# Optimization experiments

Measured on AMD Instinct MI355X. Metric: run time of the kernel, lower is better.

Reference implementation:

```python
import jax, jax.numpy as jnp
import numpy as np

N, E, F_IN, H, L = 50000, 800000, 128, 256, 3


def setup_inputs() -> dict:
    key = jax.random.key(0)
    ks = jax.random.split(key, 6)
    s = 0.05  # keep activations well-scaled through 3 residual layers
    return {
        "x": jax.random.normal(ks[0], (N, F_IN), jnp.float32),
        "edge_index": jax.random.randint(ks[1], (2, E), 0, N, dtype=jnp.int32),
        "Wp": jax.random.normal(ks[2], (H, F_IN), jnp.float32) * s,
        "bp": jnp.zeros((H,), jnp.float32),
        "Wl": jax.random.normal(ks[3], (L, H, H), jnp.float32) * s,
        "bl": jnp.zeros((L, H), jnp.float32),
        "Wr": jax.random.normal(ks[4], (L, H, H), jnp.float32) * s,
        "gamma": jnp.ones((L, H), jnp.float32),
        "beta": jnp.zeros((L, H), jnp.float32),
    }


def _layernorm(x, g, b, eps=1e-5):
    mu = jnp.mean(x, axis=-1, keepdims=True)
    var = jnp.var(x, axis=-1, keepdims=True)
    return (x - mu) * jax.lax.rsqrt(var + eps) * g + b


def reference(x, edge_index, Wp, bp, Wl, bl, Wr, gamma, beta):
    n = x.shape[0]
    src, dst = edge_index[0], edge_index[1]
    # input projection + ReLU
    h = jax.nn.relu(x @ Wp.T + bp)  # [N, H]
    # mean-aggregation normalizer (PyG SAGEConv 'mean'): zero-degree nodes -> 0
    deg = jax.ops.segment_sum(jnp.ones_like(dst, jnp.float32), dst, num_segments=n)
    inv_deg = (1.0 / jnp.maximum(deg, 1.0))[:, None]  # [N, 1]
    num_layers = Wl.shape[0]
    for i in range(num_layers):
        res = h
        # SAGEConv: lin_l(mean of source-neighbor messages) + lin_r(self)
        agg = jax.ops.segment_sum(h[src], dst, num_segments=n) * inv_deg  # [N, H]
        h = agg @ Wl[i].T + bl[i] + h @ Wr[i].T
        # LayerNorm -> ReLU -> (dropout: eval-mode identity) -> residual
        h = jax.nn.relu(_layernorm(h, gamma[i], beta[i])) + res
    return h
```

## Files before the change

kernel.cpp:

```cpp
#include <hip/hip_runtime.h>

#define NN 50000
#define EE 800000
#define FIN 128
#define HH 256
#define NL 3

#define BM 64
#define BK 32
#define ABYTES (BM*BK*2)
#define BBYTES (HH*BK*2)
#define TILEB  (ABYTES + BBYTES)
#define CSRB   782

typedef __bf16 bf16x8 __attribute__((ext_vector_type(8)));
typedef float  f32x4  __attribute__((ext_vector_type(4)));
typedef unsigned short u16x8 __attribute__((ext_vector_type(8)));

__device__ __forceinline__ float bf2f(unsigned short u){
    union { unsigned int i; float f; } v; v.i = ((unsigned int)u) << 16; return v.f;
}
__device__ __forceinline__ unsigned short f2bf(float f){
    union { float f; unsigned int i; } v; v.f = f;
    unsigned int r = v.i + 0x7FFF + ((v.i >> 16) & 1);
    return (unsigned short)(r >> 16);
}
__device__ __forceinline__ void gload16(const void* g, void* s){
    __builtin_amdgcn_global_load_lds(
        (const __attribute__((address_space(1))) void*)g,
        (__attribute__((address_space(3))) void*)s, 16, 0, 0);
}
__device__ __forceinline__ int permslot(int n){
    return (n & ~63) | ((n & 3) << 4) | ((n >> 2) & 15);
}

__global__ void k_zero_i32(int* __restrict__ p, int n){
    int i = blockIdx.x*256 + threadIdx.x;
    if (i < n) p[i] = 0;
}
__global__ void k_count_deg(const int* __restrict__ dst, int* __restrict__ deg){
    int i = blockIdx.x*256 + threadIdx.x;
    if (i < EE) atomicAdd(&deg[dst[i]], 1);
}
__global__ void k_block_sum(const int* __restrict__ deg, int* __restrict__ bsum){
    __shared__ int s[1024];
    int i = blockIdx.x*1024 + threadIdx.x;
    s[threadIdx.x] = (i < NN) ? deg[i] : 0;
    __syncthreads();
    for (int o = 512; o > 0; o >>= 1){
        if (threadIdx.x < o) s[threadIdx.x] += s[threadIdx.x + o];
        __syncthreads();
    }
    if (threadIdx.x == 0) bsum[blockIdx.x] = s[0];
}
__global__ void k_make_off(const int* __restrict__ deg, const int* __restrict__ bsum,
                           int nb, int* __restrict__ off, int* __restrict__ pos,
                           float* __restrict__ invd){
    __shared__ int s[1024];
    __shared__ int base;
    int t = threadIdx.x;
    if (t < 64){
        int v = (t < blockIdx.x && t < nb) ? bsum[t] : 0;
        #pragma unroll
        for (int m = 1; m <= 32; m <<= 1) v += __shfl_xor(v, m);
        if (t == 0) base = v;
    }
    int i = blockIdx.x*1024 + t;
    int v0 = (i < NN) ? deg[i] : 0;
    s[t] = v0; __syncthreads();
    for (int o = 1; o < 1024; o <<= 1){
        int add = (t >= o) ? s[t - o] : 0;
        __syncthreads();
        s[t] += add;
        __syncthreads();
    }
    if (i < NN){
        int excl = s[t] - v0 + base;
        off[i] = excl; pos[i] = excl;
        invd[i] = 1.0f / fmaxf((float)v0, 1.0f);
    }
}

#define NX  (NN*FIN/4)
#define NWP (HH*FIN/4)
#define NWC (NL*HH*2*HH/4)
__global__ void k_prep(const float* __restrict__ x, const float* __restrict__ Wp,
                       const float* __restrict__ Wl, const float* __restrict__ Wr,
                       unsigned short* __restrict__ Xb, unsigned short* __restrict__ Wpb,
                       unsigned short* __restrict__ Wb){
    int i = blockIdx.x*256 + threadIdx.x;
    if (i < NX){
        float4 v = *(const float4*)&x[i*4];
        ushort4 o; o.x=f2bf(v.x); o.y=f2bf(v.y); o.z=f2bf(v.z); o.w=f2bf(v.w);
        *(ushort4*)&Xb[i*4] = o;
        return;
    }
    int j = i - NX;
    if (j < NWP){
        int base = j*4;
        int kk = base & (FIN-1);
        int n  = base >> 7;
        float4 v = *(const float4*)&Wp[base];
        ushort4 o; o.x=f2bf(v.x); o.y=f2bf(v.y); o.z=f2bf(v.z); o.w=f2bf(v.w);
        *(ushort4*)&Wpb[permslot(n)*FIN + kk] = o;
        return;
    }
    int k4 = j - NWP;
    if (k4 < NWC){
        int base = k4*4;
        int kk  = base & 511;
        int n   = (base >> 9) & (HH-1);
        int lyr = base >> 17;
        const float* srcp = (kk < HH) ? &Wl[((size_t)lyr*HH + n)*HH + kk]
                                      : &Wr[((size_t)lyr*HH + n)*HH + (kk - HH)];
        float4 v = *(const float4*)srcp;
        ushort4 o; o.x=f2bf(v.x); o.y=f2bf(v.y); o.z=f2bf(v.z); o.w=f2bf(v.w);
        *(ushort4*)&Wb[(size_t)lyr*HH*2*HH + permslot(n)*2*HH + kk] = o;
    }
}

__device__ __forceinline__ void accum16(float* a, uint4 v, float c){
    const unsigned int w0 = v.x, w1 = v.y, w2 = v.z, w3 = v.w;
    #pragma unroll
    for (int b = 0; b < 4; ++b){
        a[b]    += c * (float)((w0 >> (8*b)) & 0xFF);
        a[4+b]  += c * (float)((w1 >> (8*b)) & 0xFF);
        a[8+b]  += c * (float)((w2 >> (8*b)) & 0xFF);
        a[12+b] += c * (float)((w3 >> (8*b)) & 0xFF);
    }
}

__global__ __launch_bounds__(256) void k_aggregate_u8(
    const unsigned char* __restrict__ hu, const float* __restrict__ scl,
    const int* __restrict__ csr, const int* __restrict__ off,
    const int* __restrict__ deg, const float* __restrict__ invd,
    unsigned short* __restrict__ aggb)
{
    const int wave = threadIdx.x >> 6, lane = threadIdx.x & 63;
    const int node = blockIdx.x*4 + wave;
    if (node >= NN) return;
    const int o = off[node], d = deg[node];
    const int grp = lane >> 4;
    const int fl  = lane & 15;

    float acc[16] = {};
    int j = 0;
    for (; j + 16 <= d; j += 16){
        int s0 = csr[o + j      + grp];
        int s1 = csr[o + j + 4  + grp];
        int s2 = csr[o + j + 8  + grp];
        int s3 = csr[o + j + 12 + grp];
        float c0 = scl[s0], c1 = scl[s1], c2 = scl[s2], c3 = scl[s3];
        uint4 v0 = *(const uint4*)&hu[(size_t)s0*HH + fl*16];
        uint4 v1 = *(const uint4*)&hu[(size_t)s1*HH + fl*16];
        uint4 v2 = *(const uint4*)&hu[(size_t)s2*HH + fl*16];
        uint4 v3 = *(const uint4*)&hu[(size_t)s3*HH + fl*16];
        accum16(acc, v0, c0); accum16(acc, v1, c1);
        accum16(acc, v2, c2); accum16(acc, v3, c3);
    }
    for (; j + 8 <= d; j += 8){
        int s0 = csr[o + j     + grp];
        int s1 = csr[o + j + 4 + grp];
        float c0 = scl[s0], c1 = scl[s1];
        uint4 v0 = *(const uint4*)&hu[(size_t)s0*HH + fl*16];
        uint4 v1 = *(const uint4*)&hu[(size_t)s1*HH + fl*16];
        accum16(acc, v0, c0); accum16(acc, v1, c1);
    }
    for (; j < d; j += 4){
        int idx = j + grp;
        int s0 = 0; float c0 = 0.f;
        if (idx < d){ s0 = csr[o + idx]; c0 = scl[s0]; }
        uint4 v0 = *(const uint4*)&hu[(size_t)s0*HH + fl*16];
        accum16(acc, v0, c0);
    }
    #pragma unroll
    for (int k = 0; k < 16; ++k){
        acc[k] += __shfl_xor(acc[k], 16);
        acc[k] += __shfl_xor(acc[k], 32);
    }
    if (grp == 0){
        float id = invd[node];
        u16x8 r0, r1;
        #pragma unroll
        for (int k = 0; k < 8; ++k){
            r0[k] = f2bf(acc[k]*id);
            r1[k] = f2bf(acc[8+k]*id);
        }
        *(u16x8*)&aggb[(size_t)node*HH + fl*16]     = r0;
        *(u16x8*)&aggb[(size_t)node*HH + fl*16 + 8] = r1;
    }
}

template<int EPI, bool CSR>
__global__ __launch_bounds__(512) void k_gemm_mfma(
    const unsigned short* __restrict__ A0, int lda0,
    const unsigned short* __restrict__ A1, int lda1,
    const unsigned short* __restrict__ Bt,
    const float* __restrict__ bias,
    const float* __restrict__ gamma, const float* __restrict__ beta,
    const unsigned short* __restrict__ resb,
    float* __restrict__ outf, unsigned short* __restrict__ outb,
    unsigned char* __restrict__ hu, float* __restrict__ scl,
    int K0, int KTOT, int ngemm,
    const int* __restrict__ esrc, const int* __restrict__ edst,
    int* __restrict__ pos, int* __restrict__ csr)
{
    __shared__ char smem[2*TILEB];
    if (CSR && (int)blockIdx.x >= ngemm){
        int i = ((int)blockIdx.x - ngemm)*512 + (int)threadIdx.x;
        const int stride = CSRB*512;
        for (; i < EE; i += stride){
            int p = atomicAdd(&pos[edst[i]], 1);
            csr[p] = esrc[i];
        }
        return;
    }
    const int t  = threadIdx.x;
    const int w  = t >> 6, l = t & 63;
    const int lr = l & 15, lg = l >> 4;
    const int wm = w >> 2, wn = w & 3;
    const int m0 = blockIdx.x * BM;

    const char* bsrc[2]; int bdst[2];
    #pragma unroll
    for (int i = 0; i < 2; ++i){
        int u   = t + i*512;
        int row = u >> 2;
        int swz = ((u & 3)*16) ^ ((row & 6) << 3);
        bsrc[i] = (const char*)(Bt + (size_t)row*KTOT) + swz;
        bdst[i] = ABYTES + u*16;
    }
    const int ua   = t & 255;
    const int rowA = ua >> 2;
    const int swzA = ((ua & 3)*16) ^ ((rowA & 6) << 3);
    int growA = m0 + rowA; if (growA > NN-1) growA = NN-1;
    const char* a0src = (const char*)(A0 + (size_t)growA*lda0) + swzA;
    const char* a1src = (const char*)(A1 + (size_t)growA*lda1) + swzA;
    const int adst = ua*16;
    const bool hasA = (w < 4);

    f32x4 acc[2][4] = {};

    auto stage = [&](int s, int buf){
        const int k0 = s * BK;
        char* dst = smem + buf*TILEB;
        if (hasA){
            const char* g = (k0 < K0) ? (a0src + (size_t)k0*2)
                                      : (a1src + (size_t)(k0 - K0)*2);
            gload16(g, dst + adst);
        }
        gload16(bsrc[0] + (size_t)k0*2, dst + bdst[0]);
        gload16(bsrc[1] + (size_t)k0*2, dst + bdst[1]);
    };

    const int nsteps = KTOT / BK;
    stage(0, 0);
    for (int s = 0; s < nsteps; ++s){
        const int cur = s & 1;
        if (s + 1 < nsteps){
            stage(s + 1, cur ^ 1);
            if (hasA) { asm volatile("s_waitcnt vmcnt(3)" ::: "memory"); }
            else      { asm volatile("s_waitcnt vmcnt(2)" ::: "memory"); }
        } else {
            asm volatile("s_waitcnt vmcnt(0)" ::: "memory");
        }
        __builtin_amdgcn_s_barrier();
        __builtin_amdgcn_sched_barrier(0);

        const char* As = smem + cur*TILEB;
        const char* Bs = As + ABYTES;
        const int kb = lg * 16;
        const int sw = (lr & 6) << 3;
        bf16x8 af[2], bfr[4];
        #pragma unroll
        for (int m = 0; m < 2; ++m){
            int r = wm*32 + m*16 + lr;
            af[m] = *(const bf16x8*)(As + r*64 + (kb ^ sw));
        }
        #pragma unroll
        for (int n = 0; n < 4; ++n){
            int r = wn*64 + n*16 + lr;
            bfr[n] = *(const bf16x8*)(Bs + r*64 + (kb ^ sw));
        }
        #pragma unroll
        for (int m = 0; m < 2; ++m)
            #pragma unroll
            for (int n = 0; n < 4; ++n)
                acc[m][n] = __builtin_amdgcn_mfma_f32_16x16x32_bf16(af[m], bfr[n], acc[m][n], 0, 0, 0);

        asm volatile("s_waitcnt lgkmcnt(0)" ::: "memory");
        __builtin_amdgcn_s_barrier();
    }

    const int cb = wn*64 + lr*4;
    float4 bq = *(const float4*)&bias[cb];
    float bcol[4] = {bq.x, bq.y, bq.z, bq.w};
    float gcol[4], becol[4];
    if (EPI >= 1){
        float4 gq = *(const float4*)&gamma[cb];
        float4 eq = *(const float4*)&beta[cb];
        gcol[0]=gq.x; gcol[1]=gq.y; gcol[2]=gq.z; gcol[3]=gq.w;
        becol[0]=eq.x; becol[1]=eq.y; becol[2]=eq.z; becol[3]=eq.w;
    }

    float* red  = (float*)smem;
    float* red2 = red + 512;
    float pmx[2][4];

    if (EPI == 0){
        #pragma unroll
        for (int m = 0; m < 2; ++m)
        #pragma unroll
        for (int reg = 0; reg < 4; ++reg){
            int R = wm*32 + m*16 + lg*4 + reg;
            int grow = m0 + R;
            float mx = 0.f;
            ushort4 hb4;
            #pragma unroll
            for (int n = 0; n < 4; ++n){
                float v = fmaxf(acc[m][n][reg] + bcol[n], 0.f);
                acc[m][n][reg] = v;
                mx = fmaxf(mx, v);
                ((unsigned short*)&hb4)[n] = f2bf(v);
            }
            if (grow < NN) *(ushort4*)&outb[(size_t)grow*HH + cb] = hb4;
            pmx[m][reg] = mx;
        }
    } else {
        float sm[2][4], sq[2][4];
        #pragma unroll
        for (int m = 0; m < 2; ++m)
        #pragma unroll
        for (int reg = 0; reg < 4; ++reg){
            float s = 0.f, q = 0.f;
            #pragma unroll
            for (int n = 0; n < 4; ++n){
                float v = acc[m][n][reg] + bcol[n];
                acc[m][n][reg] = v;
                s += v; q += v*v;
            }
            sm[m][reg] = s; sq[m][reg] = q;
        }
        #pragma unroll
        for (int mask = 1; mask <= 8; mask <<= 1){
            #pragma unroll
            for (int m = 0; m < 2; ++m)
            #pragma unroll
            for (int reg = 0; reg < 4; ++reg){
                sm[m][reg] += __shfl_xor(sm[m][reg], mask);
                sq[m][reg] += __shfl_xor(sq[m][reg], mask);
            }
        }
        if (lr == 0){
            #pragma unroll
            for (int m = 0; m < 2; ++m)
            #pragma unroll
            for (int reg = 0; reg < 4; ++reg){
                int R = wm*32 + m*16 + lg*4 + reg;
                red[(wn*64 + R)*2 + 0] = sm[m][reg];
                red[(wn*64 + R)*2 + 1] = sq[m][reg];
            }
        }
        __syncthreads();
        #pragma unroll
        for (int m = 0; m < 2; ++m)
        #pragma unroll
        for (int reg = 0; reg < 4; ++reg){
            int R = wm*32 + m*16 + lg*4 + reg;
            float S = 0.f, Q = 0.f;
            #pragma unroll
            for (int ww = 0; ww < 4; ++ww){
                S += red[(ww*64 + R)*2 + 0];
                Q += red[(ww*64 + R)*2 + 1];
            }
            float mean = S * (1.0f/HH);
            float var  = Q * (1.0f/HH) - mean*mean;
            float inv  = rsqrtf(var + 1e-5f);
            int grow = m0 + R;
            int growc = (grow > NN-1) ? NN-1 : grow;
            ushort4 rv = *(const ushort4*)&resb[(size_t)growc*HH + cb];
            float mx = 0.f;
            ushort4 hb4;
            f32x4 fo;
            #pragma unroll
            for (int n = 0; n < 4; ++n){
                float o = fmaxf((acc[m][n][reg] - mean)*inv*gcol[n] + becol[n], 0.f)
                          + bf2f(((const unsigned short*)&rv)[n]);
                acc[m][n][reg] = o;
                mx = fmaxf(mx, o);
                if (EPI == 1) ((unsigned short*)&hb4)[n] = f2bf(o);
                else          fo[n] = o;
            }
            if (grow < NN){
                if (EPI == 1) *(ushort4*)&outb[(size_t)grow*HH + cb] = hb4;
                else          *(f32x4*)&outf[(size_t)grow*HH + cb] = fo;
            }
            pmx[m][reg] = mx;
        }
    }

    if (EPI <= 1){
        #pragma unroll
        for (int mask = 1; mask <= 8; mask <<= 1){
            #pragma unroll
            for (int m = 0; m < 2; ++m)
            #pragma unroll
            for (int reg = 0; reg < 4; ++reg)
                pmx[m][reg] = fmaxf(pmx[m][reg], __shfl_xor(pmx[m][reg], mask));
        }
        if (EPI == 0) __syncthreads();
        if (lr == 0){
            #pragma unroll
            for (int m = 0; m < 2; ++m)
            #pragma unroll
            for (int reg = 0; reg < 4; ++reg){
                int R = wm*32 + m*16 + lg*4 + reg;
                red2[wn*64 + R] = pmx[m][reg];
            }
        }
        __syncthreads();
        #pragma unroll
        for (int m = 0; m < 2; ++m)
        #pragma unroll
        for (int reg = 0; reg < 4; ++reg){
            int R = wm*32 + m*16 + lg*4 + reg;
            float rmax = fmaxf(fmaxf(red2[R], red2[64 + R]),
                               fmaxf(red2[128 + R], red2[192 + R]));
            float qinv = (rmax > 0.f) ? (255.0f / rmax) : 0.f;
            int grow = m0 + R;
            if (grow >= NN) continue;
            unsigned int q4 = 0;
            #pragma unroll
            for (int n = 0; n < 4; ++n){
                unsigned int qv = (unsigned int)(acc[m][n][reg]*qinv + 0.5f);
                q4 |= qv << (8*n);
            }
            *(unsigned int*)&hu[(size_t)grow*HH + cb] = q4;
            if (wn == 0 && lr == 0) scl[grow] = rmax * (1.0f/255.0f);
        }
    }
}

extern "C" void kernel_launch(void* const* d_in, const int* in_sizes, int n_in,
                              void* d_out, int out_size, void* d_ws, size_t ws_size,
                              hipStream_t stream) {
    const float* x     = (const float*)d_in[0];
    const int*   ei    = (const int*)d_in[1];
    const int*   srcI  = ei;
    const int*   dstI  = ei + EE;
    const float* Wp    = (const float*)d_in[2];
    const float* bp    = (const float*)d_in[3];
    const float* Wl    = (const float*)d_in[4];
    const float* bl    = (const float*)d_in[5];
    const float* Wr    = (const float*)d_in[6];
    const float* gamma = (const float*)d_in[7];
    const float* beta  = (const float*)d_in[8];
    float* out = (float*)d_out;

    char* ws = (char*)d_ws;
    size_t off_b = 0;
    auto alloc = [&](size_t bytes) -> char* {
        char* p = ws + off_b;
        off_b = (off_b + bytes + 255) & ~(size_t)255;
        return p;
    };
    unsigned short* Hb0  = (unsigned short*)alloc((size_t)NN*HH*2);
    unsigned short* Hb1  = (unsigned short*)alloc((size_t)NN*HH*2);
    unsigned short* AGGb = (unsigned short*)alloc((size_t)NN*HH*2);
    unsigned char*  Hu0  = (unsigned char*)alloc((size_t)NN*HH);
    unsigned char*  Hu1  = (unsigned char*)alloc((size_t)NN*HH);
    float* Scl0 = (float*)alloc((size_t)NN*4);
    float* Scl1 = (float*)alloc((size_t)NN*4);
    unsigned short* Xb = (unsigned short*)alloc((size_t)NN*FIN*2);
    int*   csr  = (int*)alloc((size_t)EE*4);
    int*   deg  = (int*)alloc((size_t)NN*4);
    int*   offs = (int*)alloc((size_t)NN*4);
    int*   pos  = (int*)alloc((size_t)NN*4);
    float* invd = (float*)alloc((size_t)NN*4);
    int*   bsum = (int*)alloc(64*4);
    unsigned short* Wpb = (unsigned short*)alloc((size_t)HH*FIN*2);
    unsigned short* Wb  = (unsigned short*)alloc((size_t)NL*HH*2*HH*2);
    (void)ws_size; (void)in_sizes; (void)n_in; (void)out_size;

    const int NB = (NN + 1023)/1024;

    k_zero_i32<<<(NN + 255)/256, 256, 0, stream>>>(deg, NN);
    k_count_deg<<<(EE + 255)/256, 256, 0, stream>>>(dstI, deg);
    k_block_sum<<<NB, 1024, 0, stream>>>(deg, bsum);
    k_prep<<<(NX + NWP + NWC + 255)/256, 256, 0, stream>>>(x, Wp, Wl, Wr, Xb, Wpb, Wb);
    k_make_off<<<NB, 1024, 0, stream>>>(deg, bsum, NB, offs, pos, invd);

    const int GB = (NN + BM - 1)/BM;

    k_gemm_mfma<0,true><<<GB + CSRB, 512, 0, stream>>>(
        Xb, FIN, Xb, FIN, Wpb, bp,
        nullptr, nullptr, nullptr,
        nullptr, Hb0, Hu0, Scl0,
        FIN, FIN, GB, srcI, dstI, pos, csr);

    unsigned short* hin = Hb0;
    unsigned char*  huin = Hu0;
    float*          sclin = Scl0;
    for (int lyr = 0; lyr < NL; ++lyr){
        k_aggregate_u8<<<(NN + 3)/4, 256, 0, stream>>>(huin, sclin, csr, offs, deg,
                                                       invd, AGGb);
        unsigned short* hout  = (hin == Hb0) ? Hb1 : Hb0;
        unsigned char*  huout = (huin == Hu0) ? Hu1 : Hu0;
        float*          sclout= (sclin == Scl0) ? Scl1 : Scl0;
        const unsigned short* Wbt = Wb + (size_t)lyr*HH*2*HH;
        if (lyr < NL-1)
            k_gemm_mfma<1,false><<<GB, 512, 0, stream>>>(
                AGGb, HH, hin, HH, Wbt, bl + lyr*HH,
                gamma + lyr*HH, beta + lyr*HH, hin,
                nullptr, hout, huout, sclout,
                HH, 2*HH, GB, nullptr, nullptr, nullptr, nullptr);
        else
            k_gemm_mfma<2,false><<<GB, 512, 0, stream>>>(
                AGGb, HH, hin, HH, Wbt, bl + lyr*HH,
                gamma + lyr*HH, beta + lyr*HH, hin,
                out, nullptr, nullptr, nullptr,
                HH, 2*HH, GB, nullptr, nullptr, nullptr, nullptr);
        hin = hout; huin = huout; sclin = sclout;
    }
}
```

Measured before the change: 370.2 us.

## Store activations and aggregates as per-row uint8, dequantize A operands in registers

Drops the bf16 copies of the hidden state and the aggregate. Hidden states, residuals and aggregated features are kept only as per-row scaled uint8 and dequantized into bf16 fragments in registers inside the GEMM. The GEMM now loads its A operand directly from global memory into registers instead of staging it through LDS. The input projection reads fp32 x directly, removing the separate bf16 conversion pass. CSR construction moves out of the fused GEMM launch into its own kernel. This cuts memory traffic in the aggregate and GEMM, but adds quantization error on the residual path and the aggregates, plus per-element dequantization work in the inner loop.

```diff
diff --git a/kernel.cpp b/kernel.cpp
--- a/kernel.cpp
+++ b/kernel.cpp
@@ -8,18 +8,11 @@
 
 #define BM 64
 #define BK 32
-#define ABYTES (BM*BK*2)
 #define BBYTES (HH*BK*2)
-#define TILEB  (ABYTES + BBYTES)
-#define CSRB   782
 
 typedef __bf16 bf16x8 __attribute__((ext_vector_type(8)));
 typedef float  f32x4  __attribute__((ext_vector_type(4)));
-typedef unsigned short u16x8 __attribute__((ext_vector_type(8)));
-
-__device__ __forceinline__ float bf2f(unsigned short u){
-    union { unsigned int i; float f; } v; v.i = ((unsigned int)u) << 16; return v.f;
-}
+
 __device__ __forceinline__ unsigned short f2bf(float f){
     union { float f; unsigned int i; } v; v.f = f;
     unsigned int r = v.i + 0x7FFF + ((v.i >> 16) & 1);
@@ -80,22 +73,21 @@
         invd[i] = 1.0f / fmaxf((float)v0, 1.0f);
     }
 }
-
-#define NX  (NN*FIN/4)
+__global__ void k_build_csr(const int* __restrict__ src, const int* __restrict__ dst,
+                            int* __restrict__ pos, int* __restrict__ csr){
+    int i = blockIdx.x*256 + threadIdx.x;
+    if (i < EE){
+        int p = atomicAdd(&pos[dst[i]], 1);
+        csr[p] = src[i];
+    }
+}
+
 #define NWP (HH*FIN/4)
 #define NWC (NL*HH*2*HH/4)
-__global__ void k_prep(const float* __restrict__ x, const float* __restrict__ Wp,
+__global__ void k_prep(const float* __restrict__ Wp,
                        const float* __restrict__ Wl, const float* __restrict__ Wr,
-                       unsigned short* __restrict__ Xb, unsigned short* __restrict__ Wpb,
-                       unsigned short* __restrict__ Wb){
-    int i = blockIdx.x*256 + threadIdx.x;
-    if (i < NX){
-        float4 v = *(const float4*)&x[i*4];
-        ushort4 o; o.x=f2bf(v.x); o.y=f2bf(v.y); o.z=f2bf(v.z); o.w=f2bf(v.w);
-        *(ushort4*)&Xb[i*4] = o;
-        return;
-    }
-    int j = i - NX;
+                       unsigned short* __restrict__ Wpb, unsigned short* __restrict__ Wb){
+    int j = blockIdx.x*256 + threadIdx.x;
     if (j < NWP){
         int base = j*4;
         int kk = base & (FIN-1);
@@ -134,7 +126,7 @@
     const unsigned char* __restrict__ hu, const float* __restrict__ scl,
     const int* __restrict__ csr, const int* __restrict__ off,
     const int* __restrict__ deg, const float* __restrict__ invd,
-    unsigned short* __restrict__ aggb)
+    unsigned char* __restrict__ aggu, float* __restrict__ ascl)
 {
     const int wave = threadIdx.x >> 6, lane = threadIdx.x & 63;
     const int node = blockIdx.x*4 + wave;
@@ -178,43 +170,42 @@
         acc[k] += __shfl_xor(acc[k], 16);
         acc[k] += __shfl_xor(acc[k], 32);
     }
+    float rmax = 0.f;
+    #pragma unroll
+    for (int k = 0; k < 16; ++k) rmax = fmaxf(rmax, acc[k]);
+    #pragma unroll
+    for (int mask = 1; mask <= 8; mask <<= 1) rmax = fmaxf(rmax, __shfl_xor(rmax, mask));
+
     if (grp == 0){
-        float id = invd[node];
-        u16x8 r0, r1;
-        #pragma unroll
-        for (int k = 0; k < 8; ++k){
-            r0[k] = f2bf(acc[k]*id);
-            r1[k] = f2bf(acc[8+k]*id);
-        }
-        *(u16x8*)&aggb[(size_t)node*HH + fl*16]     = r0;
-        *(u16x8*)&aggb[(size_t)node*HH + fl*16 + 8] = r1;
-    }
-}
-
-template<int EPI, bool CSR>
+        float qinv = (rmax > 0.f) ? (255.0f / rmax) : 0.f;
+        uint4 q;
+        unsigned int* qw = (unsigned int*)&q;
+        #pragma unroll
+        for (int wi = 0; wi < 4; ++wi){
+            unsigned int pk = 0;
+            #pragma unroll
+            for (int b = 0; b < 4; ++b){
+                unsigned int qv = (unsigned int)(acc[wi*4 + b]*qinv + 0.5f);
+                pk |= qv << (8*b);
+            }
+            qw[wi] = pk;
+        }
+        *(uint4*)&aggu[(size_t)node*HH + fl*16] = q;
+        if (lane == 0) ascl[node] = rmax * invd[node] * (1.0f/255.0f);
+    }
+}
+
+template<int EPI, int ADT, int K0, int KTOT, int LDA0, int LDA1>
 __global__ __launch_bounds__(512) void k_gemm_mfma(
-    const unsigned short* __restrict__ A0, int lda0,
-    const unsigned short* __restrict__ A1, int lda1,
+    const void* __restrict__ A0v, const void* __restrict__ A1v,
+    const float* __restrict__ sA0, const float* __restrict__ sA1,
     const unsigned short* __restrict__ Bt,
     const float* __restrict__ bias,
     const float* __restrict__ gamma, const float* __restrict__ beta,
-    const unsigned short* __restrict__ resb,
-    float* __restrict__ outf, unsigned short* __restrict__ outb,
-    unsigned char* __restrict__ hu, float* __restrict__ scl,
-    int K0, int KTOT, int ngemm,
-    const int* __restrict__ esrc, const int* __restrict__ edst,
-    int* __restrict__ pos, int* __restrict__ csr)
+    const unsigned char* __restrict__ resu, const float* __restrict__ rscl,
+    float* __restrict__ outf, unsigned char* __restrict__ hu, float* __restrict__ scl)
 {
-    __shared__ char smem[2*TILEB];
-    if (CSR && (int)blockIdx.x >= ngemm){
-        int i = ((int)blockIdx.x - ngemm)*512 + (int)threadIdx.x;
-        const int stride = CSRB*512;
-        for (; i < EE; i += stride){
-            int p = atomicAdd(&pos[edst[i]], 1);
-            csr[p] = esrc[i];
-        }
-        return;
-    }
+    __shared__ char smem[2*BBYTES];
     const int t  = threadIdx.x;
     const int w  = t >> 6, l = t & 63;
     const int lr = l & 15, lg = l >> 4;
@@ -228,60 +219,112 @@
         int row = u >> 2;
         int swz = ((u & 3)*16) ^ ((row & 6) << 3);
         bsrc[i] = (const char*)(Bt + (size_t)row*KTOT) + swz;
-        bdst[i] = ABYTES + u*16;
-    }
-    const int ua   = t & 255;
-    const int rowA = ua >> 2;
-    const int swzA = ((ua & 3)*16) ^ ((rowA & 6) << 3);
-    int growA = m0 + rowA; if (growA > NN-1) growA = NN-1;
-    const char* a0src = (const char*)(A0 + (size_t)growA*lda0) + swzA;
-    const char* a1src = (const char*)(A1 + (size_t)growA*lda1) + swzA;
-    const int adst = ua*16;
-    const bool hasA = (w < 4);
+        bdst[i] = u*16;
+    }
+
+    int arow[2];
+    #pragma unroll
+    for (int m = 0; m < 2; ++m){
+        int r = m0 + wm*32 + m*16 + lr;
+        arow[m] = (r > NN-1) ? NN-1 : r;
+    }
+    float s0m[2], s1m[2];
+    if (ADT == 1){
+        #pragma unroll
+        for (int m = 0; m < 2; ++m){ s0m[m] = sA0[arow[m]]; s1m[m] = sA1[arow[m]]; }
+    }
+
+    uint2 araw[2];
+    f32x4 arf[2][2];
 
     f32x4 acc[2][4] = {};
 
-    auto stage = [&](int s, int buf){
-        const int k0 = s * BK;
-        char* dst = smem + buf*TILEB;
-        if (hasA){
-            const char* g = (k0 < K0) ? (a0src + (size_t)k0*2)
-                                      : (a1src + (size_t)(k0 - K0)*2);
-            gload16(g, dst + adst);
-        }
-        gload16(bsrc[0] + (size_t)k0*2, dst + bdst[0]);
-        gload16(bsrc[1] + (size_t)k0*2, dst + bdst[1]);
-    };
-
-    const int nsteps = KTOT / BK;
-    stage(0, 0);
+    constexpr int nsteps = KTOT / BK;
+
+    {
+        gload16(bsrc[0], smem + bdst[0]);
+        gload16(bsrc[1], smem + bdst[1]);
+        const int kk = lg*8;
+        if (ADT == 0){
+            const float* X = (const float*)A0v;
+            #pragma unroll
+            for (int m = 0; m < 2; ++m){
+                arf[m][0] = *(const f32x4*)&X[(size_t)arow[m]*LDA0 + kk];
+                arf[m][1] = *(const f32x4*)&X[(size_t)arow[m]*LDA0 + kk + 4];
+            }
+        } else {
+            #pragma unroll
+            for (int m = 0; m < 2; ++m)
+                araw[m] = *(const uint2*)((const unsigned char*)A0v + (size_t)arow[m]*LDA0 + kk);
+        }
+    }
+
+    #pragma unroll
     for (int s = 0; s < nsteps; ++s){
         const int cur = s & 1;
         if (s + 1 < nsteps){
-            stage(s + 1, cur ^ 1);
-            if (hasA) { asm volatile("s_waitcnt vmcnt(3)" ::: "memory"); }
-            else      { asm volatile("s_waitcnt vmcnt(2)" ::: "memory"); }
+            const int k0 = (s + 1) * BK;
+            char* dst = smem + (cur ^ 1)*BBYTES;
+            gload16(bsrc[0] + (size_t)k0*2, dst + bdst[0]);
+            gload16(bsrc[1] + (size_t)k0*2, dst + bdst[1]);
+            asm volatile("s_waitcnt vmcnt(2)" ::: "memory");
         } else {
             asm volatile("s_waitcnt vmcnt(0)" ::: "memory");
         }
         __builtin_amdgcn_s_barrier();
         __builtin_amdgcn_sched_barrier(0);
 
-        const char* As = smem + cur*TILEB;
-        const char* Bs = As + ABYTES;
+        bf16x8 af[2];
+        if (ADT == 0){
+            #pragma unroll
+            for (int m = 0; m < 2; ++m)
+                #pragma unroll
+                for (int j = 0; j < 4; ++j){
+                    af[m][j]   = (__bf16)arf[m][0][j];
+                    af[m][4+j] = (__bf16)arf[m][1][j];
+                }
+        } else {
+            #pragma unroll
+            for (int m = 0; m < 2; ++m){
+                const float sc = (s*BK < K0) ? s0m[m] : s1m[m];
+                #pragma unroll
+                for (int j = 0; j < 4; ++j){
+                    af[m][j]   = (__bf16)((float)((araw[m].x >> (8*j)) & 0xFF) * sc);
+                    af[m][4+j] = (__bf16)((float)((araw[m].y >> (8*j)) & 0xFF) * sc);
+                }
+            }
+        }
+
+        const char* Bs = smem + cur*BBYTES;
         const int kb = lg * 16;
         const int sw = (lr & 6) << 3;
-        bf16x8 af[2], bfr[4];
-        #pragma unroll
-        for (int m = 0; m < 2; ++m){
-            int r = wm*32 + m*16 + lr;
-            af[m] = *(const bf16x8*)(As + r*64 + (kb ^ sw));
-        }
+        bf16x8 bfr[4];
         #pragma unroll
         for (int n = 0; n < 4; ++n){
             int r = wn*64 + n*16 + lr;
             bfr[n] = *(const bf16x8*)(Bs + r*64 + (kb ^ sw));
         }
+
+        if (s + 1 < nsteps){
+            const int kk = (s + 1)*BK + lg*8;
+            if (ADT == 0){
+                const float* X = (const float*)A0v;
+                #pragma unroll
+                for (int m = 0; m < 2; ++m){
+                    arf[m][0] = *(const f32x4*)&X[(size_t)arow[m]*LDA0 + kk];
+                    arf[m][1] = *(const f32x4*)&X[(size_t)arow[m]*LDA0 + kk + 4];
+                }
+            } else {
+                #pragma unroll
+                for (int m = 0; m < 2; ++m){
+                    const unsigned char* p = (kk < K0)
+                        ? (const unsigned char*)A0v + (size_t)arow[m]*LDA0 + kk
+                        : (const unsigned char*)A1v + (size_t)arow[m]*LDA1 + (kk - K0);
+                    araw[m] = *(const uint2*)p;
+                }
+            }
+        }
+
         #pragma unroll
         for (int m = 0; m < 2; ++m)
             #pragma unroll
@@ -312,18 +355,13 @@
         for (int m = 0; m < 2; ++m)
         #pragma unroll
         for (int reg = 0; reg < 4; ++reg){
-            int R = wm*32 + m*16 + lg*4 + reg;
-            int grow = m0 + R;
             float mx = 0.f;
-            ushort4 hb4;
             #pragma unroll
             for (int n = 0; n < 4; ++n){
                 float v = fmaxf(acc[m][n][reg] + bcol[n], 0.f);
                 acc[m][n][reg] = v;
                 mx = fmaxf(mx, v);
-                ((unsigned short*)&hb4)[n] = f2bf(v);
-            }
-            if (grow < NN) *(ushort4*)&outb[(size_t)grow*HH + cb] = hb4;
+            }
             pmx[m][reg] = mx;
         }
     } else {
@@ -378,23 +416,19 @@
             float inv  = rsqrtf(var + 1e-5f);
             int grow = m0 + R;
             int growc = (grow > NN-1) ? NN-1 : grow;
-            ushort4 rv = *(const ushort4*)&resb[(size_t)growc*HH + cb];
+            unsigned int rv = *(const unsigned int*)&resu[(size_t)growc*HH + cb];
+            float rs = rscl[growc];
             float mx = 0.f;
-            ushort4 hb4;
             f32x4 fo;
             #pragma unroll
             for (int n = 0; n < 4; ++n){
                 float o = fmaxf((acc[m][n][reg] - mean)*inv*gcol[n] + becol[n], 0.f)
-                          + bf2f(((const unsigned short*)&rv)[n]);
+                          + (float)((rv >> (8*n)) & 0xFF) * rs;
                 acc[m][n][reg] = o;
                 mx = fmaxf(mx, o);
-                if (EPI == 1) ((unsigned short*)&hb4)[n] = f2bf(o);
-                else          fo[n] = o;
-            }
-            if (grow < NN){
-                if (EPI == 1) *(ushort4*)&outb[(size_t)grow*HH + cb] = hb4;
-                else          *(f32x4*)&outf[(size_t)grow*HH + cb] = fo;
-            }
+                fo[n] = o;
+            }
+            if (EPI == 2 && grow < NN) *(f32x4*)&outf[(size_t)grow*HH + cb] = fo;
             pmx[m][reg] = mx;
         }
     }
@@ -464,14 +498,12 @@
         off_b = (off_b + bytes + 255) & ~(size_t)255;
         return p;
     };
-    unsigned short* Hb0  = (unsigned short*)alloc((size_t)NN*HH*2);
-    unsigned short* Hb1  = (unsigned short*)alloc((size_t)NN*HH*2);
-    unsigned short* AGGb = (unsigned short*)alloc((size_t)NN*HH*2);
-    unsigned char*  Hu0  = (unsigned char*)alloc((size_t)NN*HH);
-    unsigned char*  Hu1  = (unsigned char*)alloc((size_t)NN*HH);
+    unsigned char* Hu0  = (unsigned char*)alloc((size_t)NN*HH);
+    unsigned char* Hu1  = (unsigned char*)alloc((size_t)NN*HH);
+    unsigned char* AGGu = (unsigned char*)alloc((size_t)NN*HH);
     float* Scl0 = (float*)alloc((size_t)NN*4);
     float* Scl1 = (float*)alloc((size_t)NN*4);
-    unsigned short* Xb = (unsigned short*)alloc((size_t)NN*FIN*2);
+    float* AScl = (float*)alloc((size_t)NN*4);
     int*   csr  = (int*)alloc((size_t)EE*4);
     int*   deg  = (int*)alloc((size_t)NN*4);
     int*   offs = (int*)alloc((size_t)NN*4);
@@ -487,39 +519,35 @@
     k_zero_i32<<<(NN + 255)/256, 256, 0, stream>>>(deg, NN);
     k_count_deg<<<(EE + 255)/256, 256, 0, stream>>>(dstI, deg);
     k_block_sum<<<NB, 1024, 0, stream>>>(deg, bsum);
-    k_prep<<<(NX + NWP + NWC + 255)/256, 256, 0, stream>>>(x, Wp, Wl, Wr, Xb, Wpb, Wb);
     k_make_off<<<NB, 1024, 0, stream>>>(deg, bsum, NB, offs, pos, invd);
+    k_prep<<<(NWP + NWC + 255)/256, 256, 0, stream>>>(Wp, Wl, Wr, Wpb, Wb);
+    k_build_csr<<<(EE + 255)/256, 256, 0, stream>>>(srcI, dstI, pos, csr);
 
     const int GB = (NN + BM - 1)/BM;
 
-    k_gemm_mfma<0,true><<<GB + CSRB, 512, 0, stream>>>(
-        Xb, FIN, Xb, FIN, Wpb, bp,
-        nullptr, nullptr, nullptr,
-        nullptr, Hb0, Hu0, Scl0,
-        FIN, FIN, GB, srcI, dstI, pos, csr);
-
-    unsigned short* hin = Hb0;
-    unsigned char*  huin = Hu0;
-    float*          sclin = Scl0;
+    k_gemm_mfma<0,0,FIN,FIN,FIN,FIN><<<GB, 512, 0, stream>>>(
+        x, x, nullptr, nullptr, Wpb, bp,
+        nullptr, nullptr, nullptr, nullptr,
+        nullptr, Hu0, Scl0);
+
+    unsigned char* huin  = Hu0;
+    float*         sclin = Scl0;
     for (int lyr = 0; lyr < NL; ++lyr){
         k_aggregate_u8<<<(NN + 3)/4, 256, 0, stream>>>(huin, sclin, csr, offs, deg,
-                                                       invd, AGGb);
-        unsigned short* hout  = (hin == Hb0) ? Hb1 : Hb0;
-        unsigned char*  huout = (huin == Hu0) ? Hu1 : Hu0;
-        float*          sclout= (sclin == Scl0) ? Scl1 : Scl0;
+                                                       invd, AGGu, AScl);
+        unsigned char* huout  = (huin == Hu0) ? Hu1 : Hu0;
+        float*         sclout = (sclin == Scl0) ? Scl1 : Scl0;
         const unsigned short* Wbt = Wb + (size_t)lyr*HH*2*HH;
         if (lyr < NL-1)
-            k_gemm_mfma<1,false><<<GB, 512, 0, stream>>>(
-                AGGb, HH, hin, HH, Wbt, bl + lyr*HH,
-                gamma + lyr*HH, beta + lyr*HH, hin,
-                nullptr, hout, huout, sclout,
-                HH, 2*HH, GB, nullptr, nullptr, nullptr, nullptr);
+            k_gemm_mfma<1,1,HH,2*HH,HH,HH><<<GB, 512, 0, stream>>>(
+                AGGu, huin, AScl, sclin, Wbt, bl + lyr*HH,
+                gamma + lyr*HH, beta + lyr*HH, huin, sclin,
+                nullptr, huout, sclout);
         else
-            k_gemm_mfma<2,false><<<GB, 512, 0, stream>>>(
-                AGGb, HH, hin, HH, Wbt, bl + lyr*HH,
-                gamma + lyr*HH, beta + lyr*HH, hin,
-                out, nullptr, nullptr, nullptr,
-                HH, 2*HH, GB, nullptr, nullptr, nullptr, nullptr);
-        hin = hout; huin = huout; sclin = sclout;
-    }
-}
+            k_gemm_mfma<2,1,HH,2*HH,HH,HH><<<GB, 512, 0, stream>>>(
+                AGGu, huin, AScl, sclin, Wbt, bl + lyr*HH,
+                gamma + lyr*HH, beta + lyr*HH, huin, sclin,
+                out, nullptr, nullptr);
+        huin = huout; sclin = sclout;
+    }
+}
```

Result: slower. 398.7 us (+7.7%).

## Double GEMM block tile to 128 rows with shared weight tile across two halves

Applied to the files above, without the earlier changes.

The GEMM kernel now runs 1024 threads per block covering 128 rows, split into two 64-row halves. Each half has its own A tile but both read a single shared B (weight) tile in LDS, so each weight chunk is loaded once per 128 rows instead of once per 64. The CSR construction that used to ride along in extra blocks of the projection GEMM moves into its own k_build_csr kernel. The trade-off is fewer blocks, higher LDS and register pressure per block, and one extra kernel launch, which also serialises CSR building with the projection GEMM.

```diff
diff --git a/kernel.cpp b/kernel.cpp
--- a/kernel.cpp
+++ b/kernel.cpp
@@ -6,12 +6,9 @@
 #define HH 256
 #define NL 3
 
-#define BM 64
+#define BM 128
 #define BK 32
-#define ABYTES (BM*BK*2)
-#define BBYTES (HH*BK*2)
-#define TILEB  (ABYTES + BBYTES)
-#define CSRB   782
+#define AOFF 32768
 
 typedef __bf16 bf16x8 __attribute__((ext_vector_type(8)));
 typedef float  f32x4  __attribute__((ext_vector_type(4)));
@@ -78,6 +75,14 @@
         int excl = s[t] - v0 + base;
         off[i] = excl; pos[i] = excl;
         invd[i] = 1.0f / fmaxf((float)v0, 1.0f);
+    }
+}
+__global__ void k_build_csr(const int* __restrict__ src, const int* __restrict__ dst,
+                            int* __restrict__ pos, int* __restrict__ csr){
+    int i = blockIdx.x*256 + threadIdx.x;
+    if (i < EE){
+        int p = atomicAdd(&pos[dst[i]], 1);
+        csr[p] = src[i];
     }
 }
 
@@ -191,8 +196,8 @@
     }
 }
 
-template<int EPI, bool CSR>
-__global__ __launch_bounds__(512) void k_gemm_mfma(
+template<int EPI>
+__global__ __launch_bounds__(1024) void k_gemm_mfma(
     const unsigned short* __restrict__ A0, int lda0,
     const unsigned short* __restrict__ A1, int lda1,
     const unsigned short* __restrict__ Bt,
@@ -201,56 +206,40 @@
     const unsigned short* __restrict__ resb,
     float* __restrict__ outf, unsigned short* __restrict__ outb,
     unsigned char* __restrict__ hu, float* __restrict__ scl,
-    int K0, int KTOT, int ngemm,
-    const int* __restrict__ esrc, const int* __restrict__ edst,
-    int* __restrict__ pos, int* __restrict__ csr)
+    int K0, int KTOT)
 {
-    __shared__ char smem[2*TILEB];
-    if (CSR && (int)blockIdx.x >= ngemm){
-        int i = ((int)blockIdx.x - ngemm)*512 + (int)threadIdx.x;
-        const int stride = CSRB*512;
-        for (; i < EE; i += stride){
-            int p = atomicAdd(&pos[edst[i]], 1);
-            csr[p] = esrc[i];
-        }
-        return;
-    }
-    const int t  = threadIdx.x;
-    const int w  = t >> 6, l = t & 63;
-    const int lr = l & 15, lg = l >> 4;
-    const int wm = w >> 2, wn = w & 3;
-    const int m0 = blockIdx.x * BM;
-
-    const char* bsrc[2]; int bdst[2];
-    #pragma unroll
-    for (int i = 0; i < 2; ++i){
-        int u   = t + i*512;
-        int row = u >> 2;
-        int swz = ((u & 3)*16) ^ ((row & 6) << 3);
-        bsrc[i] = (const char*)(Bt + (size_t)row*KTOT) + swz;
-        bdst[i] = ABYTES + u*16;
-    }
+    __shared__ char smem[AOFF + 2*8192];
+    const int t    = threadIdx.x;
+    const int w    = t >> 6, l = t & 63;
+    const int lr   = l & 15, lg = l >> 4;
+    const int half = w >> 3;
+    const int wh   = w & 7;
+    const int wm   = wh >> 2, wn = wh & 3;
+    const int m0h  = blockIdx.x * BM + half*64;
+
+    const int rowB = t >> 2;
+    const int swzB = ((t & 3)*16) ^ ((rowB & 6) << 3);
+    const char* bsrc = (const char*)(Bt + (size_t)rowB*KTOT) + swzB;
+    const int bdstB = t*16;
     const int ua   = t & 255;
     const int rowA = ua >> 2;
     const int swzA = ((ua & 3)*16) ^ ((rowA & 6) << 3);
-    int growA = m0 + rowA; if (growA > NN-1) growA = NN-1;
+    int growA = m0h + rowA; if (growA > NN-1) growA = NN-1;
     const char* a0src = (const char*)(A0 + (size_t)growA*lda0) + swzA;
     const char* a1src = (const char*)(A1 + (size_t)growA*lda1) + swzA;
-    const int adst = ua*16;
-    const bool hasA = (w < 4);
+    const int adst = AOFF + half*4096 + ua*16;
+    const bool hasA = (wh < 4);
 
     f32x4 acc[2][4] = {};
 
     auto stage = [&](int s, int buf){
         const int k0 = s * BK;
-        char* dst = smem + buf*TILEB;
         if (hasA){
             const char* g = (k0 < K0) ? (a0src + (size_t)k0*2)
                                       : (a1src + (size_t)(k0 - K0)*2);
-            gload16(g, dst + adst);
-        }
-        gload16(bsrc[0] + (size_t)k0*2, dst + bdst[0]);
-        gload16(bsrc[1] + (size_t)k0*2, dst + bdst[1]);
+            gload16(g, smem + buf*8192 + adst);
+        }
+        gload16(bsrc + (size_t)k0*2, smem + buf*16384 + bdstB);
     };
 
     const int nsteps = KTOT / BK;
@@ -259,16 +248,16 @@
         const int cur = s & 1;
         if (s + 1 < nsteps){
             stage(s + 1, cur ^ 1);
-            if (hasA) { asm volatile("s_waitcnt vmcnt(3)" ::: "memory"); }
-            else      { asm volatile("s_waitcnt vmcnt(2)" ::: "memory"); }
+            if (hasA) { asm volatile("s_waitcnt vmcnt(2)" ::: "memory"); }
+            else      { asm volatile("s_waitcnt vmcnt(1)" ::: "memory"); }
         } else {
             asm volatile("s_waitcnt vmcnt(0)" ::: "memory");
         }
         __builtin_amdgcn_s_barrier();
         __builtin_amdgcn_sched_barrier(0);
 
-        const char* As = smem + cur*TILEB;
-        const char* Bs = As + ABYTES;
+        const char* As = smem + AOFF + cur*8192 + half*4096;
+        const char* Bs = smem + cur*16384;
         const int kb = lg * 16;
         const int sw = (lr & 6) << 3;
         bf16x8 af[2], bfr[4];
@@ -303,7 +292,7 @@
         becol[0]=eq.x; becol[1]=eq.y; becol[2]=eq.z; becol[3]=eq.w;
     }
 
-    float* red  = (float*)smem;
+    float* red  = (float*)(smem + half*4096);
     float* red2 = red + 512;
     float pmx[2][4];
 
@@ -313,7 +302,7 @@
         #pragma unroll
         for (int reg = 0; reg < 4; ++reg){
             int R = wm*32 + m*16 + lg*4 + reg;
-            int grow = m0 + R;
+            int grow = m0h + R;
             float mx = 0.f;
             ushort4 hb4;
             #pragma unroll
@@ -376,7 +365,7 @@
             float mean = S * (1.0f/HH);
             float var  = Q * (1.0f/HH) - mean*mean;
             float inv  = rsqrtf(var + 1e-5f);
-            int grow = m0 + R;
+            int grow = m0h + R;
             int growc = (grow > NN-1) ? NN-1 : grow;
             ushort4 rv = *(const ushort4*)&resb[(size_t)growc*HH + cb];
             float mx = 0.f;
@@ -427,7 +416,7 @@
             float rmax = fmaxf(fmaxf(red2[R], red2[64 + R]),
                                fmaxf(red2[128 + R], red2[192 + R]));
             float qinv = (rmax > 0.f) ? (255.0f / rmax) : 0.f;
-            int grow = m0 + R;
+            int grow = m0h + R;
             if (grow >= NN) continue;
             unsigned int q4 = 0;
             #pragma unroll
@@ -487,16 +476,16 @@
     k_zero_i32<<<(NN + 255)/256, 256, 0, stream>>>(deg, NN);
     k_count_deg<<<(EE + 255)/256, 256, 0, stream>>>(dstI, deg);
     k_block_sum<<<NB, 1024, 0, stream>>>(deg, bsum);
+    k_make_off<<<NB, 1024, 0, stream>>>(deg, bsum, NB, offs, pos, invd);
     k_prep<<<(NX + NWP + NWC + 255)/256, 256, 0, stream>>>(x, Wp, Wl, Wr, Xb, Wpb, Wb);
-    k_make_off<<<NB, 1024, 0, stream>>>(deg, bsum, NB, offs, pos, invd);
+    k_build_csr<<<(EE + 255)/256, 256, 0, stream>>>(srcI, dstI, pos, csr);
 
     const int GB = (NN + BM - 1)/BM;
 
-    k_gemm_mfma<0,true><<<GB + CSRB, 512, 0, stream>>>(
-        Xb, FIN, Xb, FIN, Wpb, bp,
-        nullptr, nullptr, nullptr,
-        nullptr, Hb0, Hu0, Scl0,
-        FIN, FIN, GB, srcI, dstI, pos, csr);
+    k_gemm_mfma<0><<<GB, 1024, 0, stream>>>(Xb, FIN, Xb, FIN, Wpb, bp,
+                                            nullptr, nullptr, nullptr,
+                                            nullptr, Hb0, Hu0, Scl0,
+                                            FIN, FIN);
 
     unsigned short* hin = Hb0;
     unsigned char*  huin = Hu0;
@@ -509,17 +498,15 @@
         float*          sclout= (sclin == Scl0) ? Scl1 : Scl0;
         const unsigned short* Wbt = Wb + (size_t)lyr*HH*2*HH;
         if (lyr < NL-1)
-            k_gemm_mfma<1,false><<<GB, 512, 0, stream>>>(
-                AGGb, HH, hin, HH, Wbt, bl + lyr*HH,
-                gamma + lyr*HH, beta + lyr*HH, hin,
-                nullptr, hout, huout, sclout,
-                HH, 2*HH, GB, nullptr, nullptr, nullptr, nullptr);
+            k_gemm_mfma<1><<<GB, 1024, 0, stream>>>(AGGb, HH, hin, HH, Wbt, bl + lyr*HH,
+                                                    gamma + lyr*HH, beta + lyr*HH, hin,
+                                                    nullptr, hout, huout, sclout,
+                                                    HH, 2*HH);
         else
-            k_gemm_mfma<2,false><<<GB, 512, 0, stream>>>(
-                AGGb, HH, hin, HH, Wbt, bl + lyr*HH,
-                gamma + lyr*HH, beta + lyr*HH, hin,
-                out, nullptr, nullptr, nullptr,
-                HH, 2*HH, GB, nullptr, nullptr, nullptr, nullptr);
+            k_gemm_mfma<2><<<GB, 1024, 0, stream>>>(AGGb, HH, hin, HH, Wbt, bl + lyr*HH,
+                                                    gamma + lyr*HH, beta + lyr*HH, hin,
+                                                    out, nullptr, nullptr, nullptr,
+                                                    HH, 2*HH);
         hin = hout; huin = huout; sclin = sclout;
     }
 }
```

New measurement: 346.6 us. -6.4%, faster.
